# Kernel tuning notes

Hardware: AMD Instinct MI355X
Metric: run time of the kernel (lower is better)

Reference implementation:

```python
import jax, jax.numpy as jnp
import numpy as np

B, L, D = 4096, 50, 64
NU, NI, NR = 100000, 100000, 5


def setup_inputs() -> dict:
    key = jax.random.key(0)
    ks = jax.random.split(key, 16)
    s = 0.02
    inp = {
        "nodes_v": jax.random.randint(ks[0], (B,), 0, NI),
        "neigh_u": jax.random.randint(ks[1], (B, L), 0, NU),
        "neigh_r": jax.random.randint(ks[2], (B, L), 0, NR),
        "embed_u": jax.random.normal(ks[3], (NU, D)) * s,
        "embed_i": jax.random.normal(ks[4], (NI, D)) * s,
        "embed_r": jax.random.normal(ks[5], (NR, D)) * s,
        # gv MLP: Linear(2D,D) ReLU Linear(D,D) ReLU Linear(D,D)
        "gv_w1": jax.random.normal(ks[6], (2 * D, D)) * s, "gv_b1": jnp.zeros((D,)),
        "gv_w2": jax.random.normal(ks[7], (D, D)) * s,     "gv_b2": jnp.zeros((D,)),
        "gv_w3": jax.random.normal(ks[8], (D, D)) * s,     "gv_b3": jnp.zeros((D,)),
        # attention MLP: Linear(2D,D) ReLU Linear(D,D) ReLU Linear(D,1), softmax over neighbors
        "att_w1": jax.random.normal(ks[9], (2 * D, D)) * s, "att_b1": jnp.zeros((D,)),
        "att_w2": jax.random.normal(ks[10], (D, D)) * s,    "att_b2": jnp.zeros((D,)),
        "att_w3": jax.random.normal(ks[11], (D, 1)) * s,    "att_b3": jnp.zeros((1,)),
        # combine: Linear(2D,D) ReLU Linear(D,D) ReLU
        "wr1_w": jax.random.normal(ks[12], (2 * D, D)) * s, "wr1_b": jnp.zeros((D,)),
        "wr2_w": jax.random.normal(ks[13], (D, D)) * s,     "wr2_b": jnp.zeros((D,)),
    }
    return inp


def reference(nodes_v, neigh_u, neigh_r, embed_u, embed_i, embed_r,
              gv_w1, gv_b1, gv_w2, gv_b2, gv_w3, gv_b3,
              att_w1, att_b1, att_w2, att_b2, att_w3, att_b3,
              wr1_w, wr1_b, wr2_w, wr2_b):
    qj = embed_i[nodes_v]            # [B, D] item reps
    pt = embed_u[neigh_u]            # [B, L, D] neighbor user reps
    er = embed_r[neigh_r]            # [B, L, D] rating reps
    # fusion MLP g(.)
    x = jnp.concatenate([pt, er], axis=-1)                    # [B, L, 2D]
    h = jax.nn.relu(x @ gv_w1 + gv_b1)
    h = jax.nn.relu(h @ gv_w2 + gv_b2)
    fjt = h @ gv_w3 + gv_b3                                   # [B, L, D]
    # attention over neighbors (dropout is identity in eval mode)
    q_rep = jnp.broadcast_to(qj[:, None, :], fjt.shape)       # [B, L, D]
    a = jnp.concatenate([fjt, q_rep], axis=-1)                # [B, L, 2D]
    a = jax.nn.relu(a @ att_w1 + att_b1)
    a = jax.nn.relu(a @ att_w2 + att_b2)
    scores = (a @ att_w3 + att_b3)[..., 0]                    # [B, L]
    mu = jax.nn.softmax(scores, axis=1)                       # softmax over neighbors
    zj = jnp.einsum("bld,bl->bd", fjt, mu)                   # weighted aggregation
    # combine aggregated neighborhood with item's own embedding (2D -> D)
    z = jax.nn.relu(jnp.concatenate([zj, qj], axis=-1) @ wr1_w + wr1_b)
    out = jax.nn.relu(z @ wr2_w + wr2_b)                      # [B, D]
    return out
```

## Files before the change

kernel.cpp:

```cpp
#include <hip/hip_runtime.h>

typedef __bf16 bf16;
typedef short s16x8 __attribute__((ext_vector_type(8)));
typedef __bf16 b16x8 __attribute__((ext_vector_type(8)));
typedef float f32x4 __attribute__((ext_vector_type(4)));

#define B_   4096
#define L_   50
#define SH   72

#define OFF_W1F  0
#define OFF_W2F  8192
#define OFF_W3F  12288
#define OFF_WCF  16384
#define OFF_A2F  20480
#define OFF_R1T  24576
#define OFF_R2T  32768
#define WT_TOTAL 36864
#define BIAS1P_BYTE 73728
#define CQ_BYTE     73984

#define PREP_W_BLOCKS 145
#define PREP_C_BLOCKS 1024

__device__ __forceinline__ unsigned short f2b(float f) {
    __bf16 h = (__bf16)f;
    return __builtin_bit_cast(unsigned short, h);
}
__device__ __forceinline__ unsigned pack2(float a, float b) {
    return (unsigned)f2b(a) | ((unsigned)f2b(b) << 16);
}
__device__ __forceinline__ s16x8 mkfrag(float4 a, float4 b) {
    union { s16x8 v; unsigned u[4]; } r;
    r.u[0] = pack2(a.x, a.y); r.u[1] = pack2(a.z, a.w);
    r.u[2] = pack2(b.x, b.y); r.u[3] = pack2(b.z, b.w);
    return r.v;
}
__device__ __forceinline__ f32x4 mfma16(s16x8 a, s16x8 b, f32x4 c) {
    return __builtin_amdgcn_mfma_f32_16x16x32_bf16(a, b, c, 0, 0, 0);
}

extern "C" __global__ void prep_all(const float* __restrict__ w1, const float* __restrict__ w2,
                                    const float* __restrict__ w3, const float* __restrict__ a1,
                                    const float* __restrict__ a2, const float* __restrict__ r1,
                                    const float* __restrict__ r2, const float* __restrict__ gb3,
                                    const float* __restrict__ ab1,
                                    const int* __restrict__ nodes_v, const float* __restrict__ embed_i,
                                    bf16* __restrict__ wt, float* __restrict__ bias1p,
                                    float* __restrict__ cq)
{
    if (blockIdx.x >= PREP_W_BLOCKS) {
        int gid = (blockIdx.x - PREP_W_BLOCKS) * 256 + threadIdx.x;
        int b = gid >> 6, n = gid & 63;
        int v = nodes_v[b];
        const float* q = embed_i + v * 64;
        float s0 = 0.f, s1 = 0.f, s2 = 0.f, s3 = 0.f;
#pragma unroll
        for (int k = 0; k < 64; k += 4) {
            s0 = fmaf(q[k],     a1[(64 + k) * 64 + n],     s0);
            s1 = fmaf(q[k + 1], a1[(64 + k + 1) * 64 + n], s1);
            s2 = fmaf(q[k + 2], a1[(64 + k + 2) * 64 + n], s2);
            s3 = fmaf(q[k + 3], a1[(64 + k + 3) * 64 + n], s3);
        }
        cq[gid] = (s0 + s1) + (s2 + s3);
        return;
    }
    int i = blockIdx.x * 256 + threadIdx.x;
    if (i >= WT_TOTAL + 64) return;
    if (i >= WT_TOTAL) {
        int n = i - WT_TOTAL;
        float s0 = ab1[n], s1 = 0.f, s2 = 0.f, s3 = 0.f;
#pragma unroll
        for (int t = 0; t < 64; t += 4) {
            s0 = fmaf(gb3[t],     a1[t * 64 + n],       s0);
            s1 = fmaf(gb3[t + 1], a1[(t + 1) * 64 + n], s1);
            s2 = fmaf(gb3[t + 2], a1[(t + 2) * 64 + n], s2);
            s3 = fmaf(gb3[t + 3], a1[(t + 3) * 64 + n], s3);
        }
        bias1p[n] = (s0 + s1) + (s2 + s3);
        return;
    }
    float val;
    if (i < OFF_R1T) {
        int off, kind;
        if      (i < OFF_W2F) { off = OFF_W1F; kind = 0; }
        else if (i < OFF_W3F) { off = OFF_W2F; kind = 1; }
        else if (i < OFF_WCF) { off = OFF_W3F; kind = 2; }
        else if (i < OFF_A2F) { off = OFF_WCF; kind = 3; }
        else                  { off = OFF_A2F; kind = 4; }
        int local = i - off;
        int f = local >> 9, lane = (local >> 3) & 63, j = local & 7;
        int kt = f >> 2, nt = f & 3, quad = lane >> 4, m = lane & 15;
        int k = kt * 32 + quad * 8 + j;
        int n = nt * 16 + m;
        if (kind == 0)      val = w1[k * 64 + n];
        else if (kind == 1) val = w2[k * 64 + n];
        else if (kind == 2) val = w3[k * 64 + n];
        else if (kind == 4) val = a2[k * 64 + n];
        else {
            float s0 = 0.f, s1 = 0.f, s2 = 0.f, s3 = 0.f;
#pragma unroll
            for (int t = 0; t < 64; t += 4) {
                float4 w = *(const float4*)(w3 + k * 64 + t);
                s0 = fmaf(w.x, a1[t * 64 + n],       s0);
                s1 = fmaf(w.y, a1[(t + 1) * 64 + n], s1);
                s2 = fmaf(w.z, a1[(t + 2) * 64 + n], s2);
                s3 = fmaf(w.w, a1[(t + 3) * 64 + n], s3);
            }
            val = (s0 + s1) + (s2 + s3);
        }
    }
    else if (i < OFF_R2T) { int li = i - OFF_R1T; int n = li >> 7, k = li & 127; val = r1[k * 64 + n]; }
    else                  { int li = i - OFF_R2T; int n = li >> 6, k = li & 63;  val = r2[k * 64 + n]; }
    wt[i] = (bf16)val;
}

extern "C" __global__ void __launch_bounds__(256, 2)
dense_fused(const int* __restrict__ nodes_v, const int* __restrict__ neigh_u,
            const int* __restrict__ neigh_r,
            const float* __restrict__ embed_u, const float* __restrict__ embed_i,
            const float* __restrict__ embed_r,
            const float* __restrict__ gv_b1, const float* __restrict__ gv_b2,
            const float* __restrict__ gv_b3,
            const float* __restrict__ att_b2, const float* __restrict__ att_w3,
            const float* __restrict__ wr1_b, const float* __restrict__ wr2_b,
            const bf16* __restrict__ wt, const float* __restrict__ cq,
            const float* __restrict__ bias1p, float* __restrict__ out)
{
    __shared__ __align__(16) bf16 Ws[16384];
    __shared__ __align__(16) bf16 H[128 * SH];
    __shared__ float csS[128];
    __shared__ float qsh[128];
    __shared__ float scs[128];
    __shared__ float zp[4 * 64];

    const int tid = threadIdx.x;
    const int lane = tid & 63, wave = tid >> 6;
    const int m = lane & 15, quad = lane >> 4;
    const int b0 = blockIdx.x * 2;
    const int rw0 = wave * 32;
    const int item_w = rw0 >> 6;
    const int lbase = rw0 & 63;

    {
        const uint4* src = (const uint4*)(wt + OFF_W2F);
        uint4* dst = (uint4*)Ws;
#pragma unroll
        for (int it = 0; it < 8; ++it) dst[tid + it * 256] = src[tid + it * 256];
    }
    if (tid < 128) {
        int item = tid >> 6, n = tid & 63;
        csS[tid] = cq[(b0 + item) * 64 + n] + bias1p[n];
        qsh[tid] = embed_i[nodes_v[b0 + item] * 64 + n];
    }

    const int bw = b0 + item_w;
    const int l0 = min(lbase + m, L_ - 1);
    const int l1 = min(lbase + 16 + m, L_ - 1);
    const int u0 = neigh_u[bw * L_ + l0], u1 = neigh_u[bw * L_ + l1];
    const int v0 = neigh_r[bw * L_ + l0], v1 = neigh_r[bw * L_ + l1];

    bf16* Hw = H + rw0 * SH;
    bf16* H0 = Hw;
    bf16* H1 = Hw + 16 * SH;

    {
        const float* b00 = embed_u + u0 * 64;
        const float* b01 = embed_u + u1 * 64;
        const float* b10 = embed_r + v0 * 64;
        const float* b11 = embed_r + v1 * 64;
        f32x4 ac0[4] = {}, ac1[4] = {};
#pragma unroll
        for (int kt = 0; kt < 4; ++kt) {
            const float* s0p = (kt < 2 ? b00 : b10) + (kt & 1) * 32 + quad * 8;
            const float* s1p = (kt < 2 ? b01 : b11) + (kt & 1) * 32 + quad * 8;
            float4 a0a = *(const float4*)s0p, a0b = *(const float4*)(s0p + 4);
            float4 a1a = *(const float4*)s1p, a1b = *(const float4*)(s1p + 4);
            s16x8 a0 = mkfrag(a0a, a0b);
            s16x8 a1 = mkfrag(a1a, a1b);
#pragma unroll
            for (int nt = 0; nt < 4; ++nt) {
                s16x8 b = *(const s16x8*)(wt + OFF_W1F + (kt * 4 + nt) * 512 + lane * 8);
                ac0[nt] = mfma16(a0, b, ac0[nt]);
                ac1[nt] = mfma16(a1, b, ac1[nt]);
            }
        }
#pragma unroll
        for (int nt = 0; nt < 4; ++nt) {
            int c = nt * 16 + m;
            float bv = gv_b1[c];
#pragma unroll
            for (int r4 = 0; r4 < 4; ++r4) {
                H0[(quad * 4 + r4) * SH + c] = (bf16)fmaxf(ac0[nt][r4] + bv, 0.f);
                H1[(quad * 4 + r4) * SH + c] = (bf16)fmaxf(ac1[nt][r4] + bv, 0.f);
            }
        }
    }

    __syncthreads();

    {
        f32x4 ac0[4] = {}, ac1[4] = {};
#pragma unroll
        for (int kt = 0; kt < 2; ++kt) {
            s16x8 a0 = *(const s16x8*)(H0 + m * SH + kt * 32 + quad * 8);
            s16x8 a1 = *(const s16x8*)(H1 + m * SH + kt * 32 + quad * 8);
#pragma unroll
            for (int nt = 0; nt < 4; ++nt) {
                s16x8 b = *(const s16x8*)(Ws + (kt * 4 + nt) * 512 + lane * 8);
                ac0[nt] = mfma16(a0, b, ac0[nt]);
                ac1[nt] = mfma16(a1, b, ac1[nt]);
            }
        }
#pragma unroll
        for (int nt = 0; nt < 4; ++nt) {
            int c = nt * 16 + m;
            float bv = gv_b2[c];
#pragma unroll
            for (int r4 = 0; r4 < 4; ++r4) {
                H0[(quad * 4 + r4) * SH + c] = (bf16)fmaxf(ac0[nt][r4] + bv, 0.f);
                H1[(quad * 4 + r4) * SH + c] = (bf16)fmaxf(ac1[nt][r4] + bv, 0.f);
            }
        }
    }

    f32x4 aF0[4] = {}, aF1[4] = {};
    {
        f32x4 aA0[4] = {}, aA1[4] = {};
#pragma unroll
        for (int kt = 0; kt < 2; ++kt) {
            s16x8 a0 = *(const s16x8*)(H0 + m * SH + kt * 32 + quad * 8);
            s16x8 a1 = *(const s16x8*)(H1 + m * SH + kt * 32 + quad * 8);
#pragma unroll
            for (int nt = 0; nt < 4; ++nt) {
                s16x8 bF = *(const s16x8*)(Ws + 4096 + (kt * 4 + nt) * 512 + lane * 8);
                s16x8 bA = *(const s16x8*)(Ws + 8192 + (kt * 4 + nt) * 512 + lane * 8);
                aF0[nt] = mfma16(a0, bF, aF0[nt]);
                aF1[nt] = mfma16(a1, bF, aF1[nt]);
                aA0[nt] = mfma16(a0, bA, aA0[nt]);
                aA1[nt] = mfma16(a1, bA, aA1[nt]);
            }
        }
#pragma unroll
        for (int nt = 0; nt < 4; ++nt) {
            int c = nt * 16 + m;
            float b1v = csS[item_w * 64 + c];
#pragma unroll
            for (int r4 = 0; r4 < 4; ++r4) {
                H0[(quad * 4 + r4) * SH + c] = (bf16)fmaxf(aA0[nt][r4] + b1v, 0.f);
                H1[(quad * 4 + r4) * SH + c] = (bf16)fmaxf(aA1[nt][r4] + b1v, 0.f);
            }
        }
    }

    {
        f32x4 ac0[4] = {}, ac1[4] = {};
#pragma unroll
        for (int kt = 0; kt < 2; ++kt) {
            s16x8 a0 = *(const s16x8*)(H0 + m * SH + kt * 32 + quad * 8);
            s16x8 a1 = *(const s16x8*)(H1 + m * SH + kt * 32 + quad * 8);
#pragma unroll
            for (int nt = 0; nt < 4; ++nt) {
                s16x8 b = *(const s16x8*)(Ws + 12288 + (kt * 4 + nt) * 512 + lane * 8);
                ac0[nt] = mfma16(a0, b, ac0[nt]);
                ac1[nt] = mfma16(a1, b, ac1[nt]);
            }
        }
        float s0[4] = {0.f, 0.f, 0.f, 0.f}, s1[4] = {0.f, 0.f, 0.f, 0.f};
#pragma unroll
        for (int nt = 0; nt < 4; ++nt) {
            int c = nt * 16 + m;
            float b2v = att_b2[c], w3v = att_w3[c];
#pragma unroll
            for (int r4 = 0; r4 < 4; ++r4) {
                s0[r4] += fmaxf(ac0[nt][r4] + b2v, 0.f) * w3v;
                s1[r4] += fmaxf(ac1[nt][r4] + b2v, 0.f) * w3v;
            }
        }
#pragma unroll
        for (int mask = 1; mask < 16; mask <<= 1)
#pragma unroll
            for (int r4 = 0; r4 < 4; ++r4) {
                s0[r4] += __shfl_xor(s0[r4], mask);
                s1[r4] += __shfl_xor(s1[r4], mask);
            }
        if (m == 0) {
#pragma unroll
            for (int r4 = 0; r4 < 4; ++r4) {
                scs[item_w * 64 + lbase + quad * 4 + r4] = s0[r4];
                scs[item_w * 64 + lbase + 16 + quad * 4 + r4] = s1[r4];
            }
        }
    }
    __syncthreads();

    {
        float s = (lane < L_) ? scs[item_w * 64 + lane] : -1e30f;
        float mx = s;
#pragma unroll
        for (int off = 32; off; off >>= 1) mx = fmaxf(mx, __shfl_xor(mx, off));
        float e = (lane < L_) ? __expf(s - mx) : 0.f;
        float sum = e;
#pragma unroll
        for (int off = 32; off; off >>= 1) sum += __shfl_xor(sum, off);
        float mu = e / sum;

        float z[4] = {0.f, 0.f, 0.f, 0.f};
#pragma unroll
        for (int r4 = 0; r4 < 4; ++r4) {
            float m0 = __shfl(mu, lbase + quad * 4 + r4);
            float m1 = __shfl(mu, lbase + 16 + quad * 4 + r4);
#pragma unroll
            for (int nt = 0; nt < 4; ++nt)
                z[nt] += aF0[nt][r4] * m0 + aF1[nt][r4] * m1;
        }
#pragma unroll
        for (int nt = 0; nt < 4; ++nt) {
            z[nt] += __shfl_xor(z[nt], 16);
            z[nt] += __shfl_xor(z[nt], 32);
        }
        if (quad == 0) {
#pragma unroll
            for (int nt = 0; nt < 4; ++nt) zp[wave * 64 + nt * 16 + m] = z[nt];
        }
    }
    __syncthreads();

    if ((wave & 1) == 0) {
        const int item = wave >> 1;
        const int d = lane;
        float z = zp[wave * 64 + d] + zp[wave * 64 + 64 + d] + gv_b3[d];
        float* zsh = scs + item * 64;
        zsh[d] = z;

        float accz = wr1_b[d];
        const bf16* r1 = wt + OFF_R1T + d * 128;
#pragma unroll
        for (int k8 = 0; k8 < 8; ++k8) {
            b16x8 wv = *(const b16x8*)(r1 + k8 * 8);
#pragma unroll
            for (int j = 0; j < 8; ++j) accz = fmaf((float)wv[j], zsh[k8 * 8 + j], accz);
        }
#pragma unroll
        for (int k8 = 0; k8 < 8; ++k8) {
            b16x8 wv = *(const b16x8*)(r1 + 64 + k8 * 8);
#pragma unroll
            for (int j = 0; j < 8; ++j) accz = fmaf((float)wv[j], qsh[item * 64 + k8 * 8 + j], accz);
        }
        float* z2sh = zp + wave * 64;
        z2sh[d] = fmaxf(accz, 0.f);

        float acco = wr2_b[d];
        const bf16* r2 = wt + OFF_R2T + d * 64;
#pragma unroll
        for (int k8 = 0; k8 < 8; ++k8) {
            b16x8 wv = *(const b16x8*)(r2 + k8 * 8);
#pragma unroll
            for (int j = 0; j < 8; ++j) acco = fmaf((float)wv[j], z2sh[k8 * 8 + j], acco);
        }
        out[(b0 + item) * 64 + d] = fmaxf(acco, 0.f);
    }
}

extern "C" void kernel_launch(void* const* d_in, const int* in_sizes, int n_in,
                              void* d_out, int out_size, void* d_ws, size_t ws_size,
                              hipStream_t stream)
{
    const int* nodes_v = (const int*)d_in[0];
    const int* neigh_u = (const int*)d_in[1];
    const int* neigh_r = (const int*)d_in[2];
    const float* embed_u = (const float*)d_in[3];
    const float* embed_i = (const float*)d_in[4];
    const float* embed_r = (const float*)d_in[5];
    const float* gv_w1  = (const float*)d_in[6];  const float* gv_b1 = (const float*)d_in[7];
    const float* gv_w2  = (const float*)d_in[8];  const float* gv_b2 = (const float*)d_in[9];
    const float* gv_w3  = (const float*)d_in[10]; const float* gv_b3 = (const float*)d_in[11];
    const float* att_w1 = (const float*)d_in[12]; const float* att_b1 = (const float*)d_in[13];
    const float* att_w2 = (const float*)d_in[14]; const float* att_b2 = (const float*)d_in[15];
    const float* att_w3 = (const float*)d_in[16]; const float* att_b3 = (const float*)d_in[17];
    const float* wr1_w  = (const float*)d_in[18]; const float* wr1_b = (const float*)d_in[19];
    const float* wr2_w  = (const float*)d_in[20]; const float* wr2_b = (const float*)d_in[21];
    (void)att_b3;

    bf16*  wt     = (bf16*)d_ws;
    float* bias1p = (float*)((char*)d_ws + BIAS1P_BYTE);
    float* cq     = (float*)((char*)d_ws + CQ_BYTE);

    prep_all<<<PREP_W_BLOCKS + PREP_C_BLOCKS, 256, 0, stream>>>(
        gv_w1, gv_w2, gv_w3, att_w1, att_w2, wr1_w, wr2_w, gv_b3, att_b1,
        nodes_v, embed_i, wt, bias1p, cq);
    dense_fused<<<B_ / 2, 256, 0, stream>>>(nodes_v, neigh_u, neigh_r,
                                            embed_u, embed_i, embed_r,
                                            gv_b1, gv_b2, gv_b3, att_b2, att_w3,
                                            wr1_b, wr2_b, wt, cq, bias1p, (float*)d_out);
}
```

Baseline: 168.7 us.

## Drop LDS weight staging and use per-wave split softmax without block barriers

The block no longer copies the MLP weight tiles into shared memory; each MFMA stage reads its B fragments straight from global memory, relying on L1/L2 caching. The attention softmax becomes wave-local: each wave keeps its own max and sum and weights its partial aggregation, and the final stage merges the two halves with a rescaled, flash-style combine. This removes the 32KB weight copy, two __syncthreads, and the shared score buffer, which lowers LDS usage and synchronisation cost. The trade-off is repeated global/L1 weight fetches inside the MFMA loops in place of cheaper LDS reads.

```diff
diff --git a/kernel.cpp b/kernel.cpp
--- a/kernel.cpp
+++ b/kernel.cpp
@@ -127,12 +127,10 @@
             const bf16* __restrict__ wt, const float* __restrict__ cq,
             const float* __restrict__ bias1p, float* __restrict__ out)
 {
-    __shared__ __align__(16) bf16 Ws[16384];
     __shared__ __align__(16) bf16 H[128 * SH];
-    __shared__ float csS[128];
-    __shared__ float qsh[128];
-    __shared__ float scs[128];
     __shared__ float zp[4 * 64];
+    __shared__ float swm[4 * 2];
+    __shared__ float qsh[2 * 64];
 
     const int tid = threadIdx.x;
     const int lane = tid & 63, wave = tid >> 6;
@@ -142,23 +140,18 @@
     const int item_w = rw0 >> 6;
     const int lbase = rw0 & 63;
 
-    {
-        const uint4* src = (const uint4*)(wt + OFF_W2F);
-        uint4* dst = (uint4*)Ws;
-#pragma unroll
-        for (int it = 0; it < 8; ++it) dst[tid + it * 256] = src[tid + it * 256];
-    }
-    if (tid < 128) {
-        int item = tid >> 6, n = tid & 63;
-        csS[tid] = cq[(b0 + item) * 64 + n] + bias1p[n];
-        qsh[tid] = embed_i[nodes_v[b0 + item] * 64 + n];
-    }
-
     const int bw = b0 + item_w;
     const int l0 = min(lbase + m, L_ - 1);
     const int l1 = min(lbase + 16 + m, L_ - 1);
     const int u0 = neigh_u[bw * L_ + l0], u1 = neigh_u[bw * L_ + l1];
     const int v0 = neigh_r[bw * L_ + l0], v1 = neigh_r[bw * L_ + l1];
+
+    float cs4[4];
+#pragma unroll
+    for (int nt = 0; nt < 4; ++nt) {
+        int c = nt * 16 + m;
+        cs4[nt] = cq[bw * 64 + c] + bias1p[c];
+    }
 
     bf16* Hw = H + rw0 * SH;
     bf16* H0 = Hw;
@@ -197,8 +190,6 @@
         }
     }
 
-    __syncthreads();
-
     {
         f32x4 ac0[4] = {}, ac1[4] = {};
 #pragma unroll
@@ -207,7 +198,7 @@
             s16x8 a1 = *(const s16x8*)(H1 + m * SH + kt * 32 + quad * 8);
 #pragma unroll
             for (int nt = 0; nt < 4; ++nt) {
-                s16x8 b = *(const s16x8*)(Ws + (kt * 4 + nt) * 512 + lane * 8);
+                s16x8 b = *(const s16x8*)(wt + OFF_W2F + (kt * 4 + nt) * 512 + lane * 8);
                 ac0[nt] = mfma16(a0, b, ac0[nt]);
                 ac1[nt] = mfma16(a1, b, ac1[nt]);
             }
@@ -233,8 +224,8 @@
             s16x8 a1 = *(const s16x8*)(H1 + m * SH + kt * 32 + quad * 8);
 #pragma unroll
             for (int nt = 0; nt < 4; ++nt) {
-                s16x8 bF = *(const s16x8*)(Ws + 4096 + (kt * 4 + nt) * 512 + lane * 8);
-                s16x8 bA = *(const s16x8*)(Ws + 8192 + (kt * 4 + nt) * 512 + lane * 8);
+                s16x8 bF = *(const s16x8*)(wt + OFF_W3F + (kt * 4 + nt) * 512 + lane * 8);
+                s16x8 bA = *(const s16x8*)(wt + OFF_WCF + (kt * 4 + nt) * 512 + lane * 8);
                 aF0[nt] = mfma16(a0, bF, aF0[nt]);
                 aF1[nt] = mfma16(a1, bF, aF1[nt]);
                 aA0[nt] = mfma16(a0, bA, aA0[nt]);
@@ -244,15 +235,15 @@
 #pragma unroll
         for (int nt = 0; nt < 4; ++nt) {
             int c = nt * 16 + m;
-            float b1v = csS[item_w * 64 + c];
-#pragma unroll
-            for (int r4 = 0; r4 < 4; ++r4) {
-                H0[(quad * 4 + r4) * SH + c] = (bf16)fmaxf(aA0[nt][r4] + b1v, 0.f);
-                H1[(quad * 4 + r4) * SH + c] = (bf16)fmaxf(aA1[nt][r4] + b1v, 0.f);
-            }
-        }
-    }
-
+#pragma unroll
+            for (int r4 = 0; r4 < 4; ++r4) {
+                H0[(quad * 4 + r4) * SH + c] = (bf16)fmaxf(aA0[nt][r4] + cs4[nt], 0.f);
+                H1[(quad * 4 + r4) * SH + c] = (bf16)fmaxf(aA1[nt][r4] + cs4[nt], 0.f);
+            }
+        }
+    }
+
+    float s0[4], s1[4];
     {
         f32x4 ac0[4] = {}, ac1[4] = {};
 #pragma unroll
@@ -261,12 +252,13 @@
             s16x8 a1 = *(const s16x8*)(H1 + m * SH + kt * 32 + quad * 8);
 #pragma unroll
             for (int nt = 0; nt < 4; ++nt) {
-                s16x8 b = *(const s16x8*)(Ws + 12288 + (kt * 4 + nt) * 512 + lane * 8);
+                s16x8 b = *(const s16x8*)(wt + OFF_A2F + (kt * 4 + nt) * 512 + lane * 8);
                 ac0[nt] = mfma16(a0, b, ac0[nt]);
                 ac1[nt] = mfma16(a1, b, ac1[nt]);
             }
         }
-        float s0[4] = {0.f, 0.f, 0.f, 0.f}, s1[4] = {0.f, 0.f, 0.f, 0.f};
+#pragma unroll
+        for (int r4 = 0; r4 < 4; ++r4) { s0[r4] = 0.f; s1[r4] = 0.f; }
 #pragma unroll
         for (int nt = 0; nt < 4; ++nt) {
             int c = nt * 16 + m;
@@ -284,36 +276,35 @@
                 s0[r4] += __shfl_xor(s0[r4], mask);
                 s1[r4] += __shfl_xor(s1[r4], mask);
             }
-        if (m == 0) {
-#pragma unroll
-            for (int r4 = 0; r4 < 4; ++r4) {
-                scs[item_w * 64 + lbase + quad * 4 + r4] = s0[r4];
-                scs[item_w * 64 + lbase + 16 + quad * 4 + r4] = s1[r4];
-            }
-        }
-    }
-    __syncthreads();
-
-    {
-        float s = (lane < L_) ? scs[item_w * 64 + lane] : -1e30f;
-        float mx = s;
-#pragma unroll
-        for (int off = 32; off; off >>= 1) mx = fmaxf(mx, __shfl_xor(mx, off));
-        float e = (lane < L_) ? __expf(s - mx) : 0.f;
-        float sum = e;
-#pragma unroll
-        for (int off = 32; off; off >>= 1) sum += __shfl_xor(sum, off);
-        float mu = e / sum;
+    }
+
+    {
+        const int r0b = lbase + quad * 4;
+        float mloc = -1e30f;
+#pragma unroll
+        for (int r4 = 0; r4 < 4; ++r4) {
+            if (r0b + r4 < L_)      mloc = fmaxf(mloc, s0[r4]);
+            if (r0b + 16 + r4 < L_) mloc = fmaxf(mloc, s1[r4]);
+        }
+        mloc = fmaxf(mloc, __shfl_xor(mloc, 16));
+        mloc = fmaxf(mloc, __shfl_xor(mloc, 32));
+
+        float e0[4], e1[4], ssum = 0.f;
+#pragma unroll
+        for (int r4 = 0; r4 < 4; ++r4) {
+            e0[r4] = (r0b + r4 < L_)      ? __expf(s0[r4] - mloc) : 0.f;
+            e1[r4] = (r0b + 16 + r4 < L_) ? __expf(s1[r4] - mloc) : 0.f;
+            ssum += e0[r4] + e1[r4];
+        }
+        ssum += __shfl_xor(ssum, 16);
+        ssum += __shfl_xor(ssum, 32);
 
         float z[4] = {0.f, 0.f, 0.f, 0.f};
 #pragma unroll
-        for (int r4 = 0; r4 < 4; ++r4) {
-            float m0 = __shfl(mu, lbase + quad * 4 + r4);
-            float m1 = __shfl(mu, lbase + 16 + quad * 4 + r4);
+        for (int r4 = 0; r4 < 4; ++r4)
 #pragma unroll
             for (int nt = 0; nt < 4; ++nt)
-                z[nt] += aF0[nt][r4] * m0 + aF1[nt][r4] * m1;
-        }
+                z[nt] += aF0[nt][r4] * e0[r4] + aF1[nt][r4] * e1[r4];
 #pragma unroll
         for (int nt = 0; nt < 4; ++nt) {
             z[nt] += __shfl_xor(z[nt], 16);
@@ -323,15 +314,23 @@
 #pragma unroll
             for (int nt = 0; nt < 4; ++nt) zp[wave * 64 + nt * 16 + m] = z[nt];
         }
+        if (lane == 0) { swm[wave * 2] = ssum; swm[wave * 2 + 1] = mloc; }
     }
     __syncthreads();
 
     if ((wave & 1) == 0) {
         const int item = wave >> 1;
         const int d = lane;
-        float z = zp[wave * 64 + d] + zp[wave * 64 + 64 + d] + gv_b3[d];
-        float* zsh = scs + item * 64;
-        zsh[d] = z;
+        float ma = swm[wave * 2 + 1],      mb = swm[(wave + 1) * 2 + 1];
+        float sa = swm[wave * 2],          sb = swm[(wave + 1) * 2];
+        float M  = fmaxf(ma, mb);
+        float fa = __expf(ma - M), fb = __expf(mb - M);
+        float zj = (fa * zp[wave * 64 + d] + fb * zp[(wave + 1) * 64 + d])
+                 / (fa * sa + fb * sb) + gv_b3[d];
+
+        float* zsh = zp + wave * 64;
+        zsh[d] = zj;
+        qsh[item * 64 + d] = embed_i[nodes_v[b0 + item] * 64 + d];
 
         float accz = wr1_b[d];
         const bf16* r1 = wt + OFF_R1T + d * 128;
@@ -347,8 +346,7 @@
 #pragma unroll
             for (int j = 0; j < 8; ++j) accz = fmaf((float)wv[j], qsh[item * 64 + k8 * 8 + j], accz);
         }
-        float* z2sh = zp + wave * 64;
-        z2sh[d] = fmaxf(accz, 0.f);
+        zsh[d] = fmaxf(accz, 0.f);
 
         float acco = wr2_b[d];
         const bf16* r2 = wt + OFF_R2T + d * 64;
@@ -356,7 +354,7 @@
         for (int k8 = 0; k8 < 8; ++k8) {
             b16x8 wv = *(const b16x8*)(r2 + k8 * 8);
 #pragma unroll
-            for (int j = 0; j < 8; ++j) acco = fmaf((float)wv[j], z2sh[k8 * 8 + j], acco);
+            for (int j = 0; j < 8; ++j) acco = fmaf((float)wv[j], zsh[k8 * 8 + j], acco);
         }
         out[(b0 + item) * 64 + d] = fmaxf(acco, 0.f);
     }
```

New measurement: 167.5 us. Within noise of the previous version (-0.7%).
